# Optimization experiments

Hardware: AMD Instinct MI355X
Metric: run time of the kernel (lower is better)

Reference implementation:

```python
import jax, jax.numpy as jnp
import numpy as np
from jax import lax

VOCAB, D, H, K = 20000, 100, 100, 3
N_U, N_I, R, S, E = 256, 256, 8, 52, 20000


def _text_processor(reviews, emb_table, conv_w, conv_b):
    # reviews: [B,R,S] int -> c: [B,R,S',H]
    B, Rr, Ss = reviews.shape
    embs = emb_table[reviews]                              # [B,R,S,D]
    x = embs.reshape(B * Rr, 1, Ss, D)                     # NCHW
    c = lax.conv_general_dilated(x, conv_w, (1, 1), 'VALID',
                                 dimension_numbers=('NCHW', 'OIHW', 'NCHW'))
    c = jax.nn.relu(c + conv_b[None, :, None, None])       # [B*R,H,S',1]
    Sp = Ss - K + 1
    c = c[..., 0].transpose(0, 2, 1).reshape(B, Rr, Sp, H) # [B,R,S',H]
    return c


def _branch(reviews, emb_table, conv_w, conv_b, fc_w_w, fc_w_b, fc_w2_w, fc_w2_b):
    c = _text_processor(reviews, emb_table, conv_w, conv_b)
    rho = jax.nn.sigmoid(c @ fc_w_w.T + fc_w_b)            # [B,R,S',1]
    z = rho + lax.stop_gradient(jnp.round(rho) - rho)      # straight-through round
    z = z[..., 0]                                          # [B,R,S']
    P = jnp.max(c, axis=-2) @ fc_w2_w.T + fc_w2_b          # [B,R,D]
    return P, z


def reference(user_reviews, item_reviews, uid, iid, emb_table, conv_w, conv_b,
              fc_w_w, fc_w_b, fc_w2_w, fc_w2_b, h_r_w, h_c_w,
              user_bias, item_bias, global_bias):
    P_u, z_u = _branch(user_reviews, emb_table, conv_w, conv_b, fc_w_w, fc_w_b, fc_w2_w, fc_w2_b)
    P_i, z_i = _branch(item_reviews, emb_table, conv_w, conv_b, fc_w_w, fc_w_b, fc_w2_w, fc_w2_b)
    Pu, Pi = P_u[uid], P_i[iid]                            # edge gathers [E,R,D]
    zu, zi = z_u[uid], z_i[iid]                            # [E,R,S']
    s_uv = jnp.einsum('eud,evd->euv', Pu, Pi)              # per-edge review similarity [E,R,R]
    rho_u = jax.nn.sigmoid(s_uv.sum(-1))                   # [E,R]
    rho_v = jax.nn.sigmoid(s_uv.sum(-2))                   # [E,R]
    gamma_u_r = jnp.einsum('ers,er->es', zu, rho_u)        # [E,S']
    gamma_v_r = jnp.einsum('ers,er->es', zi, rho_v)
    pred_r = (jnp.concatenate([gamma_u_r, gamma_v_r], -1) @ h_r_w.T
              + user_bias[uid] + item_bias[iid] + global_bias)  # [E,1]
    gamma_u_c = jnp.einsum('er,erd->ed', rho_u, Pu)        # [E,D]
    gamma_v_c = jnp.einsum('er,erd->ed', rho_v, Pi)
    pred_c = jnp.concatenate([gamma_u_c, gamma_v_c], -1) @ h_c_w.T  # [E,1]
    return pred_r, pred_c, z_u, z_i


def setup_inputs() -> dict:
    key = jax.random.key(0)
    ks = jax.random.split(key, 12)
    return {
        'user_reviews': jax.random.randint(ks[0], (N_U, R, S), 0, VOCAB, dtype=jnp.int32),
        'item_reviews': jax.random.randint(ks[1], (N_I, R, S), 0, VOCAB, dtype=jnp.int32),
        'uid': jax.random.randint(ks[2], (E,), 0, N_U, dtype=jnp.int32),
        'iid': jax.random.randint(ks[3], (E,), 0, N_I, dtype=jnp.int32),
        'emb_table': jax.random.normal(ks[4], (VOCAB, D), jnp.float32) * 0.1,
        'conv_w': jax.random.normal(ks[5], (H, 1, K, D), jnp.float32) * 0.05,
        'conv_b': jnp.zeros((H,), jnp.float32),
        'fc_w_w': jax.random.normal(ks[6], (1, H), jnp.float32) * 0.1,
        'fc_w_b': jnp.zeros((1,), jnp.float32),
        'fc_w2_w': jax.random.normal(ks[7], (D, H), jnp.float32) * 0.1,
        'fc_w2_b': jnp.zeros((D,), jnp.float32),
        'h_r_w': jax.random.normal(ks[8], (1, 2 * (S - K + 1)), jnp.float32) * 0.1,
        'h_c_w': jax.random.normal(ks[9], (1, 2 * D), jnp.float32) * 0.1,
        'user_bias': jnp.zeros((N_U, 1), jnp.float32),
        'item_bias': jnp.zeros((N_I, 1), jnp.float32),
        'global_bias': jnp.zeros((1,), jnp.float32),
    }
```

## Files before the change

kernel.cpp:

```cpp
#include <hip/hip_runtime.h>
#include <hip/hip_fp16.h>
#include <math.h>


typedef __attribute__((ext_vector_type(8))) _Float16 half8;
typedef __attribute__((ext_vector_type(4))) float f32x4;

__device__ __forceinline__ float sigmoidf_(float x) { return 1.f / (1.f + expf(-x)); }
__device__ __forceinline__ ushort f2h(float x) {
    union { __half h; ushort u; } t; t.h = __float2half(x); return t.u;
}
__device__ __forceinline__ float h2f(ushort u) {
    union { __half h; ushort u; } t; t.u = u; return __half2float(t.h);
}

#define Z_MARGIN 4e-4f
#define FLAG_CAP 204800

__global__ void k_prep(const float* __restrict__ conv_w, const float* __restrict__ fc_w2_w,
                       const float* __restrict__ emb,
                       float* __restrict__ Wt, float* __restrict__ fc2t,
                       float* __restrict__ Psum, ushort* __restrict__ wpack,
                       int* __restrict__ flag_cnt, ushort* __restrict__ emb16) {
    int idx = blockIdx.x * 256 + threadIdx.x;
    if (idx < 30000) {
        int kk = idx / 100, h = idx - kk * 100;
        Wt[idx] = conv_w[h * 300 + kk];
    } else if (idx < 40000) {
        int j = idx - 30000;
        int h = j / 100, dd = j - h * 100;
        fc2t[j] = fc_w2_w[dd * 100 + h];
    } else if (idx < 91200) {
        Psum[idx - 40000] = 0.f;
    } else if (idx < 127040) {
        int j = idx - 91200;
        int frag = j >> 9, within = j & 511;
        int l = within >> 3, jj = within & 7;
        int kt = frag / 7, nt = frag % 7;
        int kk = kt * 32 + ((l >> 4) << 3) + jj;
        int h  = nt * 16 + (l & 15);
        wpack[j] = (kk < 300 && h < 100) ? f2h(conv_w[h * 300 + kk]) : (ushort)0;
    } else if (idx == 127040) {
        *flag_cnt = 0;
    } else {
        int j = idx - 127041;
        if (j < 500000) {
            float4 v = ((const float4*)emb)[j];
            uint2 o;
            o.x = (unsigned)f2h(v.x) | ((unsigned)f2h(v.y) << 16);
            o.y = (unsigned)f2h(v.z) | ((unsigned)f2h(v.w) << 16);
            ((uint2*)emb16)[j] = o;
        }
    }
}

__global__ __launch_bounds__(256, 4)
void k_branch(const int* __restrict__ u_rev, const int* __restrict__ i_rev,
              const ushort* __restrict__ emb16, const ushort* __restrict__ wpack,
              const float* __restrict__ conv_b, const float* __restrict__ fc_w_w,
              const float* __restrict__ fc_w_b, const float* __restrict__ fc_w2_b,
              const float* __restrict__ fc2t, const float* __restrict__ h_r_w,
              const float* __restrict__ h_c_w,
              float* __restrict__ Pbuf, float* __restrict__ Psum,
              float* __restrict__ zdot, float* __restrict__ Pdot,
              float* __restrict__ z_out, int* __restrict__ flag_cnt,
              int* __restrict__ flag_list) {
    __shared__ __align__(16) char smem[39840];
    ushort* xw    = (ushort*)smem;
    ushort* wbuf  = (ushort*)(smem + 26624);
    int*    s_tok = (int*)(smem + 33792);
    float*  s_vmax= (float*)(smem + 34208);
    float*  s_maxf= (float*)(smem + 37408);
    float*  s_z   = (float*)(smem + 38208);
    float*  s_lg  = (float*)(smem + 38624);
    float*  s_P   = (float*)(smem + 39040);

    const int tid = threadIdx.x, lane = tid & 63, w = tid >> 6;
    const int b = blockIdx.x;
    const int branch = b >> 10, pair = b & 1023;
    const int inst0 = pair * 2;

    const uint4* wp4 = (const uint4*)wpack;
    uint4* wbuf4 = (uint4*)wbuf;
    uint4 st0 = wp4[tid];
    uint4 st1; if (tid < 192) st1 = wp4[256 + tid];

    const int* rev = branch ? i_rev : u_rev;
    if (tid < 104) {
        int ii = tid >= 52, s = tid - ii * 52;
        s_tok[tid] = rev[(inst0 + ii) * 52 + s];
    }
    __syncthreads();

    {
        const uint2* emb2 = (const uint2*)emb16;
        uint2 v[11];
#pragma unroll
        for (int k = 0; k < 11; k++) {
            int idx = tid + (k << 8);
            if (idx < 2600) {
                int ii = idx >= 1300;
                int within = idx - ii * 1300;
                int s = within / 25, c = within - s * 25;
                v[k] = emb2[s_tok[ii * 52 + s] * 25 + c];
            }
        }
#pragma unroll
        for (int k = 0; k < 11; k++) {
            int idx = tid + (k << 8);
            if (idx < 2600) {
                int ii = idx >= 1300;
                int within = idx - ii * 1300;
                *(uint2*)(xw + ii * 6656 + within * 4) = v[k];
            }
        }
        uint4 z4; z4.x = 0u; z4.y = 0u; z4.z = 0u; z4.w = 0u;
        for (int t2 = tid; t2 < 364; t2 += 256) {
            int ii = t2 >= 182, off = t2 - ii * 182;
            ((uint4*)xw)[ii * 832 + 650 + off] = z4;
        }
    }

    wbuf4[tid] = st0;
    if (tid < 192) wbuf4[256 + tid] = st1;
    st0 = wp4[448 + tid];
    if (tid < 192) st1 = wp4[448 + 256 + tid];
    __syncthreads();

    f32x4 acc0[7], acc1[7];
#pragma unroll
    for (int nt = 0; nt < 7; nt++) {
        acc0[nt] = (f32x4){0.f, 0.f, 0.f, 0.f};
        acc1[nt] = (f32x4){0.f, 0.f, 0.f, 0.f};
    }

    const int col = lane & 15, quad = lane >> 4, q8 = quad << 3;
    const int mt = w;

    for (int kt = 0; kt < 10; kt++) {
        {
            int e0 = (mt * 16 + col) * 100 + kt * 32 + q8;
            union AU { half8 h8; uint2 u2[2]; } a0, a1;
            a0.u2[0] = *(const uint2*)(xw + e0);
            a0.u2[1] = *(const uint2*)(xw + e0 + 4);
            a1.u2[0] = *(const uint2*)(xw + 6656 + e0);
            a1.u2[1] = *(const uint2*)(xw + 6656 + e0 + 4);
#pragma unroll
            for (int nt = 0; nt < 7; nt++) {
                union BU { half8 h8; uint4 u4; } bu;
                bu.u4 = wbuf4[nt * 64 + lane];
                acc0[nt] = __builtin_amdgcn_mfma_f32_16x16x32_f16(a0.h8, bu.h8, acc0[nt], 0, 0, 0);
                acc1[nt] = __builtin_amdgcn_mfma_f32_16x16x32_f16(a1.h8, bu.h8, acc1[nt], 0, 0, 0);
            }
        }
        __syncthreads();
        if (kt < 9) {
            wbuf4[tid] = st0;
            if (tid < 192) wbuf4[256 + tid] = st1;
            if (kt < 8) {
                st0 = wp4[(kt + 2) * 448 + tid];
                if (tid < 192) st1 = wp4[(kt + 2) * 448 + 256 + tid];
            }
            __syncthreads();
        }
    }

    float cb[7], fw[7];
#pragma unroll
    for (int nt = 0; nt < 7; nt++) {
        int h = nt * 16 + col;
        cb[nt] = (h < 100) ? conv_b[h] : 0.f;
        fw[nt] = (h < 100) ? fc_w_w[h] : 0.f;
    }
    const float fcb = fc_w_b[0];

#define EPILOGUE_MM(II, ACC)                                                   \
    {                                                                          \
        float vmax[7];                                                         \
        _Pragma("unroll") for (int nt = 0; nt < 7; nt++) vmax[nt] = 0.f;       \
        _Pragma("unroll")                                                      \
        for (int j = 0; j < 4; j++) {                                          \
            int p = mt * 16 + quad * 4 + j;                                    \
            bool pv = p < 50;                                                  \
            float part = 0.f;                                                  \
            _Pragma("unroll")                                                  \
            for (int nt = 0; nt < 7; nt++) {                                   \
                float c = ACC[nt][j] + cb[nt];                                 \
                c = c > 0.f ? c : 0.f;                                         \
                part += c * fw[nt];                                            \
                if (pv) vmax[nt] = fmaxf(vmax[nt], c);                         \
            }                                                                  \
            part += __shfl_xor(part, 1, 64);                                   \
            part += __shfl_xor(part, 2, 64);                                   \
            part += __shfl_xor(part, 4, 64);                                   \
            part += __shfl_xor(part, 8, 64);                                   \
            if (pv && col == 0) {                                              \
                float logit = part + fcb;                                      \
                float z = rintf(sigmoidf_(logit));                             \
                s_z[(II) * 52 + p] = z;                                        \
                s_lg[(II) * 52 + p] = logit;                                   \
                z_out[branch * 102400 + (inst0 + (II)) * 50 + p] = z;          \
            }                                                                  \
        }                                                                      \
        _Pragma("unroll")                                                      \
        for (int nt = 0; nt < 7; nt++) {                                       \
            float m = vmax[nt];                                                \
            m = fmaxf(m, __shfl_xor(m, 16, 64));                               \
            m = fmaxf(m, __shfl_xor(m, 32, 64));                               \
            int h = nt * 16 + col;                                             \
            if (quad == 0 && h < 100) s_vmax[(II) * 400 + w * 100 + h] = m;    \
        }                                                                      \
    }

    EPILOGUE_MM(0, acc0)
    EPILOGUE_MM(1, acc1)
#undef EPILOGUE_MM
    __syncthreads();

    if (tid < 200) {
        int ii = tid >= 100, h = tid - ii * 100;
        const float* sv = s_vmax + ii * 400;
        float mx = fmaxf(fmaxf(sv[h], sv[100 + h]),
                         fmaxf(sv[200 + h], sv[300 + h]));
        s_maxf[ii * 100 + h] = mx;
    }
    __syncthreads();

    if (tid < 200) {
        int ii = tid >= 100, dd = tid - ii * 100;
        float a = fc_w2_b[dd];
        for (int h0 = 0; h0 < 100; h0 += 10) {
            float wv[10], mxv[10];
#pragma unroll
            for (int t = 0; t < 10; t++) {
                wv[t] = fc2t[(h0 + t) * 100 + dd];
                mxv[t] = s_maxf[ii * 100 + h0 + t];
            }
#pragma unroll
            for (int t = 0; t < 10; t++) a += mxv[t] * wv[t];
        }
        int inst = inst0 + ii;
        int gi = branch * 2048 + inst;
        Pbuf[gi * 100 + dd] = a;
        s_P[ii * 100 + dd] = a;
        atomicAdd(&Psum[(branch * 256 + (inst >> 3)) * 100 + dd], a);
    }
    __syncthreads();

    if (w == 0) {
#pragma unroll
        for (int ii = 0; ii < 2; ii++) {
            float v = (lane < 50) ? s_z[ii * 52 + lane] * h_r_w[branch * 50 + lane] : 0.f;
            for (int s = 1; s < 64; s <<= 1) v += __shfl_xor(v, s, 64);
            if (lane == 0) zdot[branch * 2048 + inst0 + ii] = v;
        }
    } else if (w == 1) {
#pragma unroll
        for (int ii = 0; ii < 2; ii++) {
            float u = 0.f;
            if (lane < 50) u = s_P[ii * 100 + lane] * h_c_w[branch * 100 + lane]
                             + s_P[ii * 100 + lane + 50] * h_c_w[branch * 100 + lane + 50];
            for (int s = 1; s < 64; s <<= 1) u += __shfl_xor(u, s, 64);
            if (lane == 0) Pdot[branch * 2048 + inst0 + ii] = u;
        }
    } else {
        int ii = w - 2;
        float lg = 1e9f;
        if (lane < 50) lg = s_lg[ii * 52 + lane];
        unsigned long long mb = __ballot(fabsf(lg) < Z_MARGIN);
        int cnt = __popcll(mb);
        int base = 0;
        if (lane == 0 && cnt) base = atomicAdd(flag_cnt, cnt);
        base = __shfl(base, 0, 64);
        if (fabsf(lg) < Z_MARGIN) {
            int rank = __popcll(mb & ((1ull << lane) - 1ull));
            int k = base + rank;
            if (k < FLAG_CAP) flag_list[k] = (branch * 2048 + inst0 + ii) * 50 + lane;
        }
    }
}

__launch_bounds__(256)
__global__ void k_refine(const int* __restrict__ u_rev, const int* __restrict__ i_rev,
                         const float* __restrict__ emb, const float* __restrict__ Wt,
                         const float* __restrict__ conv_b, const float* __restrict__ fc_w_w,
                         const float* __restrict__ fc_w_b, const float* __restrict__ h_r_w,
                         const int* __restrict__ flag_cnt, const int* __restrict__ flag_list,
                         float* __restrict__ z_out, float* __restrict__ zdot) {
    int n = *flag_cnt; if (n > FLAG_CAP) n = FLAG_CAP;
    const int lane = threadIdx.x & 63;
    const int wid = (blockIdx.x * 256 + threadIdx.x) >> 6;
    const int nw = gridDim.x * 4;
    const bool hv = lane < 50;
    const float cb0 = hv ? conv_b[lane] : 0.f;
    const float cb1 = hv ? conv_b[lane + 50] : 0.f;
    const float fw0 = hv ? fc_w_w[lane] : 0.f;
    const float fw1 = hv ? fc_w_w[lane + 50] : 0.f;
    const float fcb = fc_w_b[0];

    for (int e0 = wid * 4; e0 < n; e0 += nw * 4) {
        int gi[4], pos[4];
        bool iv[4];
        float xr[4][5];
#pragma unroll
        for (int m = 0; m < 4; m++) {
            int e = e0 + m;
            iv[m] = e < n;
            int code = iv[m] ? flag_list[e] : 0;
            gi[m] = code / 50; pos[m] = code - gi[m] * 50;
            const int* rev = (gi[m] >> 11) ? i_rev : u_rev;
            int tb = (gi[m] & 2047) * 52 + pos[m];
            int t0 = rev[tb], t1 = rev[tb + 1], t2 = rev[tb + 2];
#pragma unroll
            for (int s = 0; s < 5; s++) {
                int k = s * 64 + lane;
                float v = 0.f;
                if (k < 300) {
                    int r = k / 100, dd = k - r * 100;
                    int t = (r == 0) ? t0 : ((r == 1) ? t1 : t2);
                    v = emb[t * 100 + dd];
                }
                xr[m][s] = v;
            }
        }
        float c0[4], c1[4];
#pragma unroll
        for (int m = 0; m < 4; m++) { c0[m] = cb0; c1[m] = cb1; }
        for (int s = 0; s < 5; s++) {
            const int dmax = (s < 4) ? 64 : 44;
            for (int db = 0; db < dmax; db += 16) {
                const int cnt = (dmax - db < 16) ? (dmax - db) : 16;
                float w0a[16], w1a[16];
#pragma unroll
                for (int t = 0; t < 16; t++) {
                    int d = s * 64 + db + t;
                    bool on = (t < cnt) && hv;
                    w0a[t] = on ? Wt[d * 100 + lane] : 0.f;
                    w1a[t] = on ? Wt[d * 100 + lane + 50] : 0.f;
                }
#pragma unroll
                for (int t = 0; t < 16; t++) {
#pragma unroll
                    for (int m = 0; m < 4; m++) {
                        float x = __shfl(xr[m][s], db + t, 64);
                        c0[m] += x * w0a[t];
                        c1[m] += x * w1a[t];
                    }
                }
            }
        }
#pragma unroll
        for (int m = 0; m < 4; m++) {
            float v = fmaxf(c0[m], 0.f) * fw0 + fmaxf(c1[m], 0.f) * fw1;
            for (int s = 1; s < 64; s <<= 1) v += __shfl_xor(v, s, 64);
            if (lane == 0 && iv[m]) {
                int branch = gi[m] >> 11, inst = gi[m] & 2047;
                float z = rintf(sigmoidf_(v + fcb));
                float old = z_out[branch * 102400 + inst * 50 + pos[m]];
                if (z != old) {
                    z_out[branch * 102400 + inst * 50 + pos[m]] = z;
                    atomicAdd(&zdot[gi[m]], (z - old) * h_r_w[branch * 50 + pos[m]]);
                }
            }
        }
    }
}

__launch_bounds__(256)
__global__ void k_gmat(const float* __restrict__ Pbuf, const float* __restrict__ Psum,
                       ushort* __restrict__ G) {
    __shared__ __align__(16) float sv[100];
    const int b = blockIdx.x, s = b >> 11, i = (b >> 3) & 255, jc = b & 7;
    const int tid = threadIdx.x, lane = tid & 63, w = tid >> 6;
    const float* vec = Psum + (s == 0 ? 25600 : 0) + i * 100;
    if (tid < 100) sv[tid] = vec[tid];
    __syncthreads();
    const int g = lane >> 2, q = lane & 3;
    const float4* rows4 = (const float4*)(Pbuf + s * 204800);
    const float4* sv4 = (const float4*)sv;
    for (int pass = 0; pass < 4; pass++) {
        int j = jc * 256 + pass * 64 + w * 16 + g;
        float part = 0.f;
#pragma unroll
        for (int t = 0; t < 7; t++) {
            int c = q + 4 * t;
            if (c < 25) {
                float4 a = rows4[j * 25 + c], bb = sv4[c];
                part += a.x * bb.x + a.y * bb.y + a.z * bb.z + a.w * bb.w;
            }
        }
        part += __shfl_xor(part, 1, 64);
        part += __shfl_xor(part, 2, 64);
        if (q == 0) G[s * 524288 + i * 2048 + j] = f2h(part);
    }
}

__launch_bounds__(256)
__global__ void k_edge(const int* __restrict__ uid, const int* __restrict__ iid,
                       const ushort* __restrict__ G,
                       const float* __restrict__ zdot, const float* __restrict__ Pdot,
                       const float* __restrict__ user_bias, const float* __restrict__ item_bias,
                       const float* __restrict__ global_bias, float* __restrict__ out) {
    const int tid = threadIdx.x, lane = tid & 63, w = tid >> 6;
    const int e = blockIdx.x * 16 + w * 4 + (lane >> 4);
    const int r = lane & 15;
    int u = uid[e], i = iid[e];
    float gv, wr, wc;
    if (r < 8) {
        gv = h2f(G[i * 2048 + u * 8 + r]);
        wr = zdot[u * 8 + r]; wc = Pdot[u * 8 + r];
    } else {
        int a = r - 8;
        gv = h2f(G[524288 + u * 2048 + i * 8 + a]);
        wr = zdot[2048 + i * 8 + a]; wc = Pdot[2048 + i * 8 + a];
    }
    float sg = sigmoidf_(gv);
    float cr = sg * wr, cc = sg * wc;
    cr += __shfl_xor(cr, 1, 64); cc += __shfl_xor(cc, 1, 64);
    cr += __shfl_xor(cr, 2, 64); cc += __shfl_xor(cc, 2, 64);
    cr += __shfl_xor(cr, 4, 64); cc += __shfl_xor(cc, 4, 64);
    cr += __shfl_xor(cr, 8, 64); cc += __shfl_xor(cc, 8, 64);
    if (r == 0) {
        out[e] = cr + user_bias[u] + item_bias[i] + global_bias[0];
        out[20000 + e] = cc;
    }
}

extern "C" void kernel_launch(void* const* d_in, const int* in_sizes, int n_in,
                              void* d_out, int out_size, void* d_ws, size_t ws_size,
                              hipStream_t stream) {
    const int*   u_rev    = (const int*)d_in[0];
    const int*   i_rev    = (const int*)d_in[1];
    const int*   uid      = (const int*)d_in[2];
    const int*   iid      = (const int*)d_in[3];
    const float* emb      = (const float*)d_in[4];
    const float* conv_w   = (const float*)d_in[5];
    const float* conv_b   = (const float*)d_in[6];
    const float* fc_w_w   = (const float*)d_in[7];
    const float* fc_w_b   = (const float*)d_in[8];
    const float* fc_w2_w  = (const float*)d_in[9];
    const float* fc_w2_b  = (const float*)d_in[10];
    const float* h_r_w    = (const float*)d_in[11];
    const float* h_c_w    = (const float*)d_in[12];
    const float* user_b   = (const float*)d_in[13];
    const float* item_b   = (const float*)d_in[14];
    const float* global_b = (const float*)d_in[15];
    float* out = (float*)d_out;

    float*  ws    = (float*)d_ws;
    float*  Pbuf  = ws;
    float*  Psum  = ws + 409600;
    float*  zdotb = ws + 460800;
    float*  Pdotb = ws + 464896;
    float*  Wt    = ws + 468992;
    float*  fc2t  = ws + 498992;
    ushort* wpack = (ushort*)(ws + 508992);
    int*    flagc = (int*)(ws + 526912);
    int*    flist = (int*)(ws + 526916);
    ushort* emb16 = (ushort*)(ws + 731716);
    ushort* Gbuf  = (ushort*)(ws + 1731716);

    hipLaunchKernelGGL(k_prep, dim3(2450), dim3(256), 0, stream,
                       conv_w, fc_w2_w, emb, Wt, fc2t, Psum, wpack, flagc, emb16);
    hipLaunchKernelGGL(k_branch, dim3(2048), dim3(256), 0, stream,
                       u_rev, i_rev, emb16, wpack, conv_b, fc_w_w, fc_w_b,
                       fc_w2_b, fc2t, h_r_w, h_c_w,
                       Pbuf, Psum, zdotb, Pdotb, out + 40000, flagc, flist);
    hipLaunchKernelGGL(k_refine, dim3(128), dim3(256), 0, stream,
                       u_rev, i_rev, emb, Wt, conv_b, fc_w_w, fc_w_b, h_r_w,
                       flagc, flist, out + 40000, zdotb);
    hipLaunchKernelGGL(k_gmat, dim3(4096), dim3(256), 0, stream, Pbuf, Psum, Gbuf);
    hipLaunchKernelGGL(k_edge, dim3(1250), dim3(256), 0, stream,
                       uid, iid, Gbuf, zdotb, Pdotb,
                       user_b, item_b, global_b, out);
}
```

Before: 184.9 us.

## Move max-pooled fc_w2 projection out of branch kernel into MFMA GEMM kernel

The per-instance 100x100 fp32 projection of max-pooled conv features, along with the Psum atomics and Pdot reduction, is taken out of k_branch. k_branch now writes half-precision max features to a padded buffer. A new k_proj kernel runs this projection as an fp16 MFMA GEMM over all 4096 instances, writing Pbuf, Pdot and group sums directly without atomics. This shortens k_branch and cuts its shared memory, at the cost of an extra launch, an extra global round trip, and fp16 rounding of the P inputs.

Measured after the change: 190.2 us. 2.9% more time.

```diff
diff --git a/kernel.cpp b/kernel.cpp
--- a/kernel.cpp
+++ b/kernel.cpp
@@ -21,7 +21,8 @@
                        const float* __restrict__ emb,
                        float* __restrict__ Wt, float* __restrict__ fc2t,
                        float* __restrict__ Psum, ushort* __restrict__ wpack,
-                       int* __restrict__ flag_cnt, ushort* __restrict__ emb16) {
+                       int* __restrict__ flag_cnt, ushort* __restrict__ emb16,
+                       ushort* __restrict__ fc2pack) {
     int idx = blockIdx.x * 256 + threadIdx.x;
     if (idx < 30000) {
         int kk = idx / 100, h = idx - kk * 100;
@@ -50,6 +51,16 @@
             o.x = (unsigned)f2h(v.x) | ((unsigned)f2h(v.y) << 16);
             o.y = (unsigned)f2h(v.z) | ((unsigned)f2h(v.w) << 16);
             ((uint2*)emb16)[j] = o;
+        } else {
+            int j2 = j - 500000;
+            if (j2 < 14336) {
+                int frag = j2 >> 9, within = j2 & 511;
+                int l = within >> 3, jj = within & 7;
+                int kt = frag / 7, nt = frag % 7;
+                int k = kt * 32 + ((l >> 4) << 3) + jj;
+                int n = nt * 16 + (l & 15);
+                fc2pack[j2] = (k < 100 && n < 100) ? f2h(fc_w2_w[n * 100 + k]) : (ushort)0;
+            }
         }
     }
 }
@@ -58,22 +69,17 @@
 void k_branch(const int* __restrict__ u_rev, const int* __restrict__ i_rev,
               const ushort* __restrict__ emb16, const ushort* __restrict__ wpack,
               const float* __restrict__ conv_b, const float* __restrict__ fc_w_w,
-              const float* __restrict__ fc_w_b, const float* __restrict__ fc_w2_b,
-              const float* __restrict__ fc2t, const float* __restrict__ h_r_w,
-              const float* __restrict__ h_c_w,
-              float* __restrict__ Pbuf, float* __restrict__ Psum,
-              float* __restrict__ zdot, float* __restrict__ Pdot,
-              float* __restrict__ z_out, int* __restrict__ flag_cnt,
-              int* __restrict__ flag_list) {
-    __shared__ __align__(16) char smem[39840];
+              const float* __restrict__ fc_w_b, const float* __restrict__ h_r_w,
+              float* __restrict__ zdot, float* __restrict__ z_out,
+              int* __restrict__ flag_cnt, int* __restrict__ flag_list,
+              ushort* __restrict__ Maxf16) {
+    __shared__ __align__(16) char smem[38240];
     ushort* xw    = (ushort*)smem;
     ushort* wbuf  = (ushort*)(smem + 26624);
     int*    s_tok = (int*)(smem + 33792);
     float*  s_vmax= (float*)(smem + 34208);
-    float*  s_maxf= (float*)(smem + 37408);
-    float*  s_z   = (float*)(smem + 38208);
-    float*  s_lg  = (float*)(smem + 38624);
-    float*  s_P   = (float*)(smem + 39040);
+    float*  s_z   = (float*)(smem + 37408);
+    float*  s_lg  = (float*)(smem + 37824);
 
     const int tid = threadIdx.x, lane = tid & 63, w = tid >> 6;
     const int b = blockIdx.x;
@@ -222,47 +228,18 @@
         const float* sv = s_vmax + ii * 400;
         float mx = fmaxf(fmaxf(sv[h], sv[100 + h]),
                          fmaxf(sv[200 + h], sv[300 + h]));
-        s_maxf[ii * 100 + h] = mx;
-    }
-    __syncthreads();
-
-    if (tid < 200) {
-        int ii = tid >= 100, dd = tid - ii * 100;
-        float a = fc_w2_b[dd];
-        for (int h0 = 0; h0 < 100; h0 += 10) {
-            float wv[10], mxv[10];
-#pragma unroll
-            for (int t = 0; t < 10; t++) {
-                wv[t] = fc2t[(h0 + t) * 100 + dd];
-                mxv[t] = s_maxf[ii * 100 + h0 + t];
-            }
-#pragma unroll
-            for (int t = 0; t < 10; t++) a += mxv[t] * wv[t];
-        }
-        int inst = inst0 + ii;
-        int gi = branch * 2048 + inst;
-        Pbuf[gi * 100 + dd] = a;
-        s_P[ii * 100 + dd] = a;
-        atomicAdd(&Psum[(branch * 256 + (inst >> 3)) * 100 + dd], a);
-    }
-    __syncthreads();
-
-    if (w == 0) {
-#pragma unroll
-        for (int ii = 0; ii < 2; ii++) {
-            float v = (lane < 50) ? s_z[ii * 52 + lane] * h_r_w[branch * 50 + lane] : 0.f;
-            for (int s = 1; s < 64; s <<= 1) v += __shfl_xor(v, s, 64);
-            if (lane == 0) zdot[branch * 2048 + inst0 + ii] = v;
-        }
-    } else if (w == 1) {
-#pragma unroll
-        for (int ii = 0; ii < 2; ii++) {
-            float u = 0.f;
-            if (lane < 50) u = s_P[ii * 100 + lane] * h_c_w[branch * 100 + lane]
-                             + s_P[ii * 100 + lane + 50] * h_c_w[branch * 100 + lane + 50];
-            for (int s = 1; s < 64; s <<= 1) u += __shfl_xor(u, s, 64);
-            if (lane == 0) Pdot[branch * 2048 + inst0 + ii] = u;
-        }
+        Maxf16[(branch * 2048 + inst0 + ii) * 128 + h] = f2h(mx);
+    } else {
+        int t = tid - 200;
+        int ii = t >= 28, h = 100 + t - ii * 28;
+        Maxf16[(branch * 2048 + inst0 + ii) * 128 + h] = (ushort)0;
+    }
+
+    if (w == 0 || w == 1) {
+        int ii = w;
+        float v = (lane < 50) ? s_z[ii * 52 + lane] * h_r_w[branch * 50 + lane] : 0.f;
+        for (int s = 1; s < 64; s <<= 1) v += __shfl_xor(v, s, 64);
+        if (lane == 0) zdot[branch * 2048 + inst0 + ii] = v;
     } else {
         int ii = w - 2;
         float lg = 1e9f;
@@ -276,6 +253,74 @@
             int rank = __popcll(mb & ((1ull << lane) - 1ull));
             int k = base + rank;
             if (k < FLAG_CAP) flag_list[k] = (branch * 2048 + inst0 + ii) * 50 + lane;
+        }
+    }
+}
+
+__launch_bounds__(256)
+__global__ void k_proj(const ushort* __restrict__ Maxf16, const ushort* __restrict__ fc2pack,
+                       const float* __restrict__ fc_w2_b, const float* __restrict__ h_c_w,
+                       float* __restrict__ Pbuf, float* __restrict__ Psum,
+                       float* __restrict__ Pdot) {
+    const int tid = threadIdx.x, lane = tid & 63, w = tid >> 6;
+    const int blk = blockIdx.x;
+    const int col = lane & 15, quad = lane >> 4, q8 = quad << 3;
+    const int arow = blk * 64 + w * 16 + col;
+    const int branch = blk >> 5;
+
+    const uint4* fp4 = (const uint4*)fc2pack;
+    f32x4 acc[7];
+#pragma unroll
+    for (int nt = 0; nt < 7; nt++) acc[nt] = (f32x4){0.f, 0.f, 0.f, 0.f};
+
+    for (int kt = 0; kt < 4; kt++) {
+        union AU { half8 h8; uint4 u4; } a;
+        a.u4 = *(const uint4*)(Maxf16 + arow * 128 + kt * 32 + q8);
+#pragma unroll
+        for (int nt = 0; nt < 7; nt++) {
+            union BU { half8 h8; uint4 u4; } bu;
+            bu.u4 = fp4[kt * 448 + nt * 64 + lane];
+            acc[nt] = __builtin_amdgcn_mfma_f32_16x16x32_f16(a.h8, bu.h8, acc[nt], 0, 0, 0);
+        }
+    }
+
+    float bias[7], hcv[7], psum_part[7];
+#pragma unroll
+    for (int nt = 0; nt < 7; nt++) {
+        int dd = nt * 16 + col;
+        bias[nt] = (dd < 100) ? fc_w2_b[dd] : 0.f;
+        hcv[nt]  = (dd < 100) ? h_c_w[branch * 100 + dd] : 0.f;
+        psum_part[nt] = 0.f;
+    }
+
+#pragma unroll
+    for (int j = 0; j < 4; j++) {
+        int inst = blk * 64 + w * 16 + quad * 4 + j;
+        float pd = 0.f;
+#pragma unroll
+        for (int nt = 0; nt < 7; nt++) {
+            int dd = nt * 16 + col;
+            float p = acc[nt][j] + bias[nt];
+            if (dd < 100) Pbuf[inst * 100 + dd] = p;
+            pd += p * hcv[nt];
+            psum_part[nt] += p;
+        }
+        pd += __shfl_xor(pd, 1, 64);
+        pd += __shfl_xor(pd, 2, 64);
+        pd += __shfl_xor(pd, 4, 64);
+        pd += __shfl_xor(pd, 8, 64);
+        if (col == 0) Pdot[inst] = pd;
+    }
+
+#pragma unroll
+    for (int nt = 0; nt < 7; nt++)
+        psum_part[nt] += __shfl_xor(psum_part[nt], 16, 64);
+    if ((quad & 1) == 0) {
+        int g = blk * 8 + w * 2 + (quad >> 1);
+#pragma unroll
+        for (int nt = 0; nt < 7; nt++) {
+            int dd = nt * 16 + col;
+            if (dd < 100) Psum[g * 100 + dd] = psum_part[nt];
         }
     }
 }
@@ -459,13 +504,17 @@
     int*    flist = (int*)(ws + 526916);
     ushort* emb16 = (ushort*)(ws + 731716);
     ushort* Gbuf  = (ushort*)(ws + 1731716);
-
-    hipLaunchKernelGGL(k_prep, dim3(2450), dim3(256), 0, stream,
-                       conv_w, fc_w2_w, emb, Wt, fc2t, Psum, wpack, flagc, emb16);
+    ushort* Maxf16  = (ushort*)(ws + 2256008);
+    ushort* fc2pack = (ushort*)(ws + 2518152);
+
+    hipLaunchKernelGGL(k_prep, dim3(2506), dim3(256), 0, stream,
+                       conv_w, fc_w2_w, emb, Wt, fc2t, Psum, wpack, flagc, emb16,
+                       fc2pack);
     hipLaunchKernelGGL(k_branch, dim3(2048), dim3(256), 0, stream,
                        u_rev, i_rev, emb16, wpack, conv_b, fc_w_w, fc_w_b,
-                       fc_w2_b, fc2t, h_r_w, h_c_w,
-                       Pbuf, Psum, zdotb, Pdotb, out + 40000, flagc, flist);
+                       h_r_w, zdotb, out + 40000, flagc, flist, Maxf16);
+    hipLaunchKernelGGL(k_proj, dim3(64), dim3(256), 0, stream,
+                       Maxf16, fc2pack, fc_w2_b, h_c_w, Pbuf, Psum, Pdotb);
     hipLaunchKernelGGL(k_refine, dim3(128), dim3(256), 0, stream,
                        u_rev, i_rev, emb, Wt, conv_b, fc_w_w, fc_w_b, h_r_w,
                        flagc, flist, out + 40000, zdotb);
```

## Compute G matrix with tiled fp16 MFMA instead of per-row dot products

Applied to the files above, without the earlier changes.

k_gmat is rewritten as a tiled GEMM: each block loads a 64x100 tile from Psum and a 64x100 tile from Pbuf into shared memory as fp16, zero-padded to K=128, then computes a 64x64 output tile with mfma_f32_16x16x32_f16. This replaces 4096 blocks of scalar float4 dot products that reread the Pbuf rows for every i, aiming to reuse loaded tiles and use matrix cores. The inputs are now rounded to fp16 before multiplying, which loses some precision compared with the previous fp32 products. The grid shrinks to 256 blocks.

Result: faster. 172.3 us, median of 2 (-6.8%).

```diff
diff --git a/kernel.cpp b/kernel.cpp
--- a/kernel.cpp
+++ b/kernel.cpp
@@ -369,29 +369,62 @@
 __launch_bounds__(256)
 __global__ void k_gmat(const float* __restrict__ Pbuf, const float* __restrict__ Psum,
                        ushort* __restrict__ G) {
-    __shared__ __align__(16) float sv[100];
-    const int b = blockIdx.x, s = b >> 11, i = (b >> 3) & 255, jc = b & 7;
+    __shared__ __align__(16) ushort Af[64 * 136];
+    __shared__ __align__(16) ushort Bf[64 * 136];
+
     const int tid = threadIdx.x, lane = tid & 63, w = tid >> 6;
-    const float* vec = Psum + (s == 0 ? 25600 : 0) + i * 100;
-    if (tid < 100) sv[tid] = vec[tid];
+    const int b = blockIdx.x;
+    const int s = b >> 7, it = (b >> 5) & 3, jt = b & 31;
+    const int ibase = it * 64, jbase = jt * 64;
+
+    const float4* psum4 = (const float4*)(Psum + (s == 0 ? 25600 : 0) + ibase * 100);
+    const float4* pbuf4 = (const float4*)(Pbuf + (s * 2048 + jbase) * 100);
+
+    for (int g = tid; g < 3200; g += 256) {
+        int side = g >= 1600, within = g - side * 1600;
+        int r = within / 25, c4 = within - r * 25;
+        float4 v = side ? pbuf4[r * 25 + c4] : psum4[r * 25 + c4];
+        uint2 o;
+        o.x = (unsigned)f2h(v.x) | ((unsigned)f2h(v.y) << 16);
+        o.y = (unsigned)f2h(v.z) | ((unsigned)f2h(v.w) << 16);
+        ushort* dst = (side ? Bf : Af) + r * 136 + c4 * 4;
+        *(uint2*)dst = o;
+    }
+    for (int t = tid; t < 896; t += 256) {
+        int side = t >= 448, within = t - side * 448;
+        int r = within / 7, k = within - r * 7;
+        ushort* dst = (side ? Bf : Af) + r * 136 + 100 + k * 4;
+        *(uint2*)dst = (uint2){0u, 0u};
+    }
     __syncthreads();
-    const int g = lane >> 2, q = lane & 3;
-    const float4* rows4 = (const float4*)(Pbuf + s * 204800);
-    const float4* sv4 = (const float4*)sv;
-    for (int pass = 0; pass < 4; pass++) {
-        int j = jc * 256 + pass * 64 + w * 16 + g;
-        float part = 0.f;
-#pragma unroll
-        for (int t = 0; t < 7; t++) {
-            int c = q + 4 * t;
-            if (c < 25) {
-                float4 a = rows4[j * 25 + c], bb = sv4[c];
-                part += a.x * bb.x + a.y * bb.y + a.z * bb.z + a.w * bb.w;
-            }
-        }
-        part += __shfl_xor(part, 1, 64);
-        part += __shfl_xor(part, 2, 64);
-        if (q == 0) G[s * 524288 + i * 2048 + j] = f2h(part);
+
+    const int col = lane & 15, quad = lane >> 4, q8 = quad << 3;
+
+    f32x4 acc[4];
+#pragma unroll
+    for (int nt = 0; nt < 4; nt++) acc[nt] = (f32x4){0.f, 0.f, 0.f, 0.f};
+
+#pragma unroll
+    for (int kt = 0; kt < 4; kt++) {
+        union FU { half8 h8; uint4 u4; } a;
+        a.u4 = *(const uint4*)(Af + (w * 16 + col) * 136 + kt * 32 + q8);
+#pragma unroll
+        for (int nt = 0; nt < 4; nt++) {
+            union FU bu;
+            bu.u4 = *(const uint4*)(Bf + (nt * 16 + col) * 136 + kt * 32 + q8);
+            acc[nt] = __builtin_amdgcn_mfma_f32_16x16x32_f16(a.h8, bu.h8, acc[nt], 0, 0, 0);
+        }
+    }
+
+    ushort* Gs = G + s * 524288;
+#pragma unroll
+    for (int nt = 0; nt < 4; nt++) {
+#pragma unroll
+        for (int jj = 0; jj < 4; jj++) {
+            int gi_row = ibase + w * 16 + quad * 4 + jj;
+            int gj = jbase + nt * 16 + col;
+            Gs[gi_row * 2048 + gj] = f2h(acc[nt][jj]);
+        }
     }
 }
 
@@ -469,7 +502,7 @@
     hipLaunchKernelGGL(k_refine, dim3(128), dim3(256), 0, stream,
                        u_rev, i_rev, emb, Wt, conv_b, fc_w_w, fc_w_b, h_r_w,
                        flagc, flist, out + 40000, zdotb);
-    hipLaunchKernelGGL(k_gmat, dim3(4096), dim3(256), 0, stream, Pbuf, Psum, Gbuf);
+    hipLaunchKernelGGL(k_gmat, dim3(256), dim3(256), 0, stream, Pbuf, Psum, Gbuf);
     hipLaunchKernelGGL(k_edge, dim3(1250), dim3(256), 0, stream,
                        uid, iid, Gbuf, zdotb, Pdotb,
                        user_b, item_b, global_b, out);
```
